# Kernel tuning notes

Hardware: AMD Instinct MI355X
Metric: run time of the kernel (lower is better)

The kernel has to match this reference:

```python
import jax, jax.numpy as jnp
import numpy as np

N_EMBD = 1024
N_HEAD = 16

def setup_inputs() -> dict:
    key = jax.random.key(0)
    ks = jax.random.split(key, 5)
    s = 0.02
    return {
        "x": jax.random.normal(ks[0], (4, 2048, N_EMBD), dtype=jnp.float32),
        "w_attn": jax.random.normal(ks[1], (N_EMBD, 3 * N_EMBD), dtype=jnp.float32) * s,
        "b_attn": jnp.zeros((3 * N_EMBD,), dtype=jnp.float32),
        "w_proj": jax.random.normal(ks[2], (N_EMBD, N_EMBD), dtype=jnp.float32) * s,
        "b_proj": jnp.zeros((N_EMBD,), dtype=jnp.float32),
    }

def reference(x, w_attn, b_attn, w_proj, b_proj):
    B, T, C = x.shape
    H = N_HEAD
    D = C // H
    qkv = x @ w_attn + b_attn                       # [B,T,3C]
    q, k, v = jnp.split(qkv, 3, axis=-1)
    # [B,H,T,D]
    q = q.reshape(B, T, H, D).transpose(0, 2, 1, 3)
    k = k.reshape(B, T, H, D).transpose(0, 2, 1, 3)
    v = v.reshape(B, T, H, D).transpose(0, 2, 1, 3)
    scale = 1.0 / jnp.sqrt(jnp.asarray(D, dtype=x.dtype))
    attn = jnp.einsum("bhqd,bhkd->bhqk", q, k) * scale
    mask = jnp.tril(jnp.ones((T, T), dtype=bool))
    attn = jnp.where(mask, attn, jnp.asarray(-jnp.inf, dtype=attn.dtype))
    attn = jax.nn.softmax(attn, axis=-1)
    out = jnp.einsum("bhqk,bhkd->bhqd", attn, v)    # [B,H,T,D]
    out = out.transpose(0, 2, 1, 3).reshape(B, T, C)
    return out @ w_proj + b_proj
```

## Files before the change

### kernel.cpp

```cpp
#include <hip/hip_runtime.h>


typedef unsigned short u16b;
typedef __bf16 bf16x8 __attribute__((ext_vector_type(8)));
typedef float f32x4 __attribute__((ext_vector_type(4)));
typedef float f32x16 __attribute__((ext_vector_type(16)));
typedef unsigned short u16x4 __attribute__((ext_vector_type(4)));

#define AS1(p) ((const __attribute__((address_space(1))) void*)(p))
#define AS3(p) ((__attribute__((address_space(3))) void*)(p))
#define GLDS(g, l) __builtin_amdgcn_global_load_lds(AS1(g), AS3(l), 16, 0, 0)

__device__ __forceinline__ u16b bfr(float v) {
  union { float f; unsigned u; } x; x.f = v;
  unsigned r = x.u + 0x7fffu + ((x.u >> 16) & 1u);
  return (u16b)(r >> 16);
}

__device__ __forceinline__ unsigned pk2(float lo, float hi) {
  union { __bf16 h[2]; unsigned u; } t;
  t.h[0] = (__bf16)lo; t.h[1] = (__bf16)hi;
  return t.u;
}

__device__ __forceinline__ float max16(const f32x16& v) {
  float a0 = fmaxf(v[0], v[1]), a1 = fmaxf(v[2], v[3]);
  float a2 = fmaxf(v[4], v[5]), a3 = fmaxf(v[6], v[7]);
  float b0 = fmaxf(v[8], v[9]), b1 = fmaxf(v[10], v[11]);
  float b2 = fmaxf(v[12], v[13]), b3 = fmaxf(v[14], v[15]);
  float c0 = fmaxf(a0, a1), c1 = fmaxf(a2, a3);
  float c2 = fmaxf(b0, b1), c3 = fmaxf(b2, b3);
  return fmaxf(fmaxf(c0, c1), fmaxf(c2, c3));
}

__device__ __forceinline__ float sum16(const f32x16& v) {
  float a0 = v[0] + v[1], a1 = v[2] + v[3], a2 = v[4] + v[5], a3 = v[6] + v[7];
  float b0 = v[8] + v[9], b1 = v[10] + v[11], b2 = v[12] + v[13], b3 = v[14] + v[15];
  float c0 = a0 + a1, c1 = a2 + a3, c2 = b0 + b1, c3 = b2 + b3;
  return (c0 + c1) + (c2 + c3);
}

__global__ __launch_bounds__(256) void cvt_bf16_kernel(
    const float* __restrict__ src, u16b* __restrict__ dst, int n4) {
  int i = blockIdx.x * 256 + threadIdx.x;
  const int stride = gridDim.x * 256;
  for (; i < n4; i += stride) {
    const float4 v = reinterpret_cast<const float4*>(src)[i];
    u16x4 o;
    o[0] = bfr(v.x); o[1] = bfr(v.y); o[2] = bfr(v.z); o[3] = bfr(v.w);
    reinterpret_cast<u16x4*>(dst)[i] = o;
  }
}

__global__ __launch_bounds__(256) void transpose_cvt_kernel(
    const float* __restrict__ src, u16b* __restrict__ dst, int R, int C) {
  __shared__ u16b tile[64][72];
  const int nc = C >> 6;
  const int br = blockIdx.x / nc, bc = blockIdx.x % nc;
  const int r0 = br << 6, c0 = bc << 6;
  const int c = threadIdx.x & 63, r4 = threadIdx.x >> 6;
  #pragma unroll
  for (int i = 0; i < 16; ++i) {
    const int r = r4 + 4 * i;
    tile[r][c] = bfr(src[(size_t)(r0 + r) * C + c0 + c]);
  }
  __syncthreads();
  #pragma unroll
  for (int i = 0; i < 16; ++i) {
    const int rr = r4 + 4 * i;
    dst[(size_t)(c0 + rr) * R + r0 + c] = tile[c][rr];
  }
}

template <int EPI>
__global__ __launch_bounds__(256, 2) void gemm128_kernel(
    const u16b* __restrict__ A, const u16b* __restrict__ Bt,
    const float* __restrict__ bias,
    u16b* __restrict__ oQ, u16b* __restrict__ oK, u16b* __restrict__ oVt,
    float* __restrict__ oF, int M, int N, int K) {
  __shared__ u16b smem[16384];
  const int tid = threadIdx.x;
  const int wid = tid >> 6, lane = tid & 63;
  const int nb = N >> 7;
  const int lin = (blockIdx.x & 7) * ((int)gridDim.x >> 3) + (blockIdx.x >> 3);
  const int brow = lin / nb, bcol = lin % nb;
  const int wr = (wid >> 1) << 6, wc = (wid & 1) << 6;

  f32x4 acc[4][4] = {};

  const int ar = (wid << 4) + (lane >> 2);
  const int acs = (((lane & 3) ^ ((lane >> 3) & 3))) << 3;
  const u16b* Ab = A + (size_t)((brow << 7) + ar) * K + acs;
  const u16b* Bb = Bt + (size_t)((bcol << 7) + ar) * K + acs;
  const int fr = lane & 15;
  const int pcs = (((lane >> 4) ^ ((fr >> 1) & 3))) << 4;
  const int nk = K >> 5;

#define STAGE(bufi, kk)                                                        \
  {                                                                            \
    char* sb = (char*)smem + (bufi) * 16384;                                   \
    GLDS(Ab + (kk),                  sb + wid * 1024);                         \
    GLDS(Ab + (size_t)64 * K + (kk), sb + 4096 + wid * 1024);                  \
    GLDS(Bb + (kk),                  sb + 8192 + wid * 1024);                  \
    GLDS(Bb + (size_t)64 * K + (kk), sb + 12288 + wid * 1024);                 \
  }

  STAGE(0, 0);
  STAGE(1, 32);

  #pragma unroll 1
  for (int kt = 0; kt < nk; ++kt) {
    if (kt + 1 < nk) asm volatile("s_waitcnt vmcnt(4)" ::: "memory");
    else             asm volatile("s_waitcnt vmcnt(0)" ::: "memory");
    __builtin_amdgcn_s_barrier();

    const char* As = (const char*)smem + (kt & 1) * 16384;
    const char* Bs = As + 8192;
    bf16x8 af[4], bfv[4];
    #pragma unroll
    for (int i = 0; i < 4; ++i)
      af[i] = *(const bf16x8*)(As + (wr + i * 16 + fr) * 64 + pcs);
    #pragma unroll
    for (int j = 0; j < 4; ++j)
      bfv[j] = *(const bf16x8*)(Bs + (wc + j * 16 + fr) * 64 + pcs);
    __builtin_amdgcn_s_setprio(1);
    #pragma unroll
    for (int i = 0; i < 4; ++i)
      #pragma unroll
      for (int j = 0; j < 4; ++j)
        acc[i][j] = __builtin_amdgcn_mfma_f32_16x16x32_bf16(af[i], bfv[j], acc[i][j], 0, 0, 0);
    __builtin_amdgcn_s_setprio(0);

    __builtin_amdgcn_s_barrier();
    if (kt + 2 < nk) STAGE(kt & 1, (kt + 2) << 5);
  }
#undef STAGE

  const int fq = lane >> 4;
  if (EPI == 1) {
    #pragma unroll
    for (int j = 0; j < 4; ++j) {
      const int n0 = (bcol << 7) + wc + j * 16 + fr;
      const float bv = bias[n0];
      #pragma unroll
      for (int i = 0; i < 4; ++i) {
        #pragma unroll
        for (int r = 0; r < 4; ++r) {
          const int m0 = (brow << 7) + wr + i * 16 + fq * 4 + r;
          oF[(size_t)m0 * N + n0] = acc[i][j][r] + bv;
        }
      }
    }
  } else {
    const int sect = bcol >> 3;
    if (sect < 2) {
      const float qs = (sect == 0) ? 0.1803368801f : 1.0f;
      u16b* oPtr = (sect == 0) ? oQ : oK;
      u16b* tile = (u16b*)smem;
      #pragma unroll
      for (int j = 0; j < 4; ++j) {
        const int n = wc + j * 16 + fr;
        const float bv = bias[(bcol << 7) + n];
        #pragma unroll
        for (int i = 0; i < 4; ++i) {
          #pragma unroll
          for (int r = 0; r < 4; ++r) {
            const int m = wr + i * 16 + fq * 4 + r;
            const int byteoff = m * 256 + (((n >> 3) ^ (m & 7)) << 4) + ((n & 7) << 1);
            *(u16b*)((char*)tile + byteoff) = bfr((acc[i][j][r] + bv) * qs);
          }
        }
      }
      __syncthreads();
      const int nh = wid >> 1;
      const int c = lane & 7;
      #pragma unroll
      for (int it = 0; it < 8; ++it) {
        const int m = ((wid & 1) << 6) + (it << 3) + (lane >> 3);
        const int chunk = (nh << 3) + (c ^ (m & 7));
        const bf16x8 val = *(const bf16x8*)((const char*)tile + m * 256 + chunk * 16);
        const int m0 = (brow << 7) + m;
        const int n0 = (bcol << 7) + (nh << 6) + (c << 3);
        const int bb = m0 >> 11, tt = m0 & 2047;
        const int h = (n0 >> 6) & 15, d = n0 & 63;
        *(bf16x8*)(oPtr + (((size_t)(bb * 16 + h) * 2048 + tt) * 64 + d)) = val;
      }
    } else {
      u16b* tile = (u16b*)smem;
      #pragma unroll
      for (int j = 0; j < 4; ++j) {
        const int nl = wc + j * 16 + fr;
        const float bv = bias[(bcol << 7) + nl];
        #pragma unroll
        for (int i = 0; i < 4; ++i) {
          #pragma unroll
          for (int r = 0; r < 4; ++r) {
            const int m = wr + i * 16 + fq * 4 + r;
            const int byteoff = nl * 256 + (((m >> 3) ^ (nl & 7)) << 4) + ((m & 7) << 1);
            *(u16b*)((char*)tile + byteoff) = bfr(acc[i][j][r] + bv);
          }
        }
      }
      __syncthreads();
      const int row0 = wid << 5;
      const int c16 = lane & 15;
      const int rr = lane >> 4;
      const int t0 = (brow << 7) & 2047;
      const int bb = brow >> 4;
      #pragma unroll
      for (int it = 0; it < 8; ++it) {
        const int nl = row0 + (it << 2) + rr;
        const int pch = c16 ^ (nl & 7);
        const bf16x8 val = *(const bf16x8*)((const char*)tile + nl * 256 + pch * 16);
        const int h = ((bcol & 7) << 1) + (nl >> 6);
        const int d = nl & 63;
        *(bf16x8*)(oVt + ((size_t)((bb << 4) + h) * 64 + d) * 2048 + t0 + (c16 << 3)) = val;
      }
    }
  }
}

__global__ __launch_bounds__(256, 2) void flash_kernel(
    const u16b* __restrict__ Q, const u16b* __restrict__ K,
    const u16b* __restrict__ Vt, u16b* __restrict__ O) {
  __shared__ u16b smem[32768];
  const int bid = blockIdx.x;
  const int bh = bid & 63;
  const int dp = bid >> 6;
  const int p = (dp < 4) ? dp : (11 - dp);
  const int g1 = p, g2 = 15 - p;
  const int tid = threadIdx.x, wid = tid >> 6, lane = tid & 63;
  const int ln31 = lane & 31, hi = lane >> 5;
  const int l7 = ln31 & 7;
  const size_t baseQK = (size_t)bh * 2048 * 64;
  const size_t baseV = (size_t)bh * 64 * 2048;
  const int b = bh >> 4, h = bh & 15;
  const int rk = lane >> 3;
  const int sk = ((lane & 7) ^ rk) << 3;
  const int rv = lane >> 4;
  const int cv = lane & 15;

#define FSTAGE(kt, bi)                                                         \
  {                                                                            \
    char* kb_ = (char*)smem + (bi) * 32768;                                    \
    char* vb_ = kb_ + 16384;                                                   \
    const int k0_ = (kt) << 7;                                                 \
    _Pragma("unroll")                                                          \
    for (int c = 0; c < 4; ++c) {                                              \
      const int i = 4 * wid + c;                                               \
      const int r = 8 * i + rk;                                                \
      GLDS(K + baseQK + (size_t)(k0_ + r) * 64 + sk, kb_ + i * 1024);          \
    }                                                                          \
    _Pragma("unroll")                                                          \
    for (int c = 0; c < 4; ++c) {                                              \
      const int i = 4 * wid + c;                                               \
      const int r = 4 * i + rv;                                                \
      const int scv = (cv ^ (r & 7)) << 3;                                     \
      GLDS(Vt + baseV + (size_t)r * 2048 + k0_ + scv, vb_ + i * 1024);         \
    }                                                                          \
  }

  const int q0wA = (g1 << 7) + wid * 32;
  const int q0wB = (g2 << 7) + wid * 32;

  bf16x8 qfA[4], qfB[4];
  {
    const u16b* qpA = Q + baseQK + (size_t)(q0wA + ln31) * 64 + hi * 8;
    const u16b* qpB = Q + baseQK + (size_t)(q0wB + ln31) * 64 + hi * 8;
    #pragma unroll
    for (int kk = 0; kk < 4; ++kk) {
      qfA[kk] = *(const bf16x8*)(qpA + kk * 16);
      qfB[kk] = *(const bf16x8*)(qpB + kk * 16);
    }
  }

  float mA = -3e38f, lA = 0.f, mB = -3e38f, lB = 0.f;
  f32x16 oaA0 = {}, oaA1 = {}, oaB0 = {}, oaB1 = {};

  FSTAGE(0, 0);
  FSTAGE(1, 1);

  #pragma unroll 1
  for (int kt = 0; kt <= g2; ++kt) {
    if (kt < g2) asm volatile("s_waitcnt vmcnt(8)" ::: "memory");
    else         asm volatile("s_waitcnt vmcnt(0)" ::: "memory");
    __builtin_amdgcn_s_barrier();

    const char* kb = (const char*)smem + (kt & 1) * 32768;
    const char* vb = kb + 16384;

    auto compute_tile = [&](const bf16x8* qf, float& m_run, float& l_run,
                            f32x16& oa0, f32x16& oa1, const int gq) {
      const bool diag = (kt == gq);
      const int maxsub = diag ? wid : 3;

      f32x16 s[4] = {};
      __builtin_amdgcn_s_setprio(1);
      #pragma unroll
      for (int ss = 0; ss < 4; ++ss) {
        if (ss <= maxsub) {
          const int row = 32 * ss + ln31;
          #pragma unroll
          for (int kk = 0; kk < 4; ++kk) {
            const int ch = (2 * kk + hi) ^ l7;
            const bf16x8 kf = *(const bf16x8*)(kb + row * 128 + ch * 16);
            s[ss] = __builtin_amdgcn_mfma_f32_32x32x16_bf16(kf, qf[kk], s[ss], 0, 0, 0);
          }
        }
      }
      __builtin_amdgcn_s_setprio(0);

      if (diag) {
        #pragma unroll
        for (int ss = 0; ss < 4; ++ss) {
          if (ss == wid) {
            #pragma unroll
            for (int r = 0; r < 16; ++r) {
              const int kvr = (r & 3) + 8 * (r >> 2) + 4 * hi;
              if (kvr > ln31) s[ss][r] = -3e38f;
            }
          }
        }
      }

      float tm = -3e38f;
      #pragma unroll
      for (int ss = 0; ss < 4; ++ss)
        if (ss <= maxsub) tm = fmaxf(tm, max16(s[ss]));
      tm = fmaxf(tm, __shfl_xor(tm, 32));

      if (!__all(tm <= m_run + 8.f)) {
        const float mnew = fmaxf(m_run, tm);
        const float scale = __builtin_amdgcn_exp2f(m_run - mnew);
        m_run = mnew;
        l_run *= scale;
        #pragma unroll
        for (int r = 0; r < 16; ++r) { oa0[r] *= scale; oa1[r] *= scale; }
      }

      float rs = 0.f;
      #pragma unroll
      for (int ss = 0; ss < 4; ++ss) {
        if (ss <= maxsub) {
          #pragma unroll
          for (int r = 0; r < 16; ++r)
            s[ss][r] = __builtin_amdgcn_exp2f(s[ss][r] - m_run);
          rs += sum16(s[ss]);
        }
      }
      rs += __shfl_xor(rs, 32);
      l_run += rs;

      union WB { unsigned u[4]; bf16x8 v; };
      __builtin_amdgcn_s_setprio(1);
      #pragma unroll
      for (int ss = 0; ss < 4; ++ss) {
        if (ss <= maxsub) {
          WB pA, pB;
#define MKPA(W0, W1, W2, W3, P0, P1, P2, P3, P4, P5, P6, P7)                 \
          {                                                                   \
            unsigned a0 = pk2(P0, P1), a1 = pk2(P2, P3);                      \
            unsigned b0 = pk2(P4, P5), b1 = pk2(P6, P7);                      \
            auto r0 = __builtin_amdgcn_permlane32_swap(a0, b0, false, false); \
            auto r1 = __builtin_amdgcn_permlane32_swap(a1, b1, false, false); \
            unsigned o0[2], o1[2];                                            \
            __builtin_memcpy(o0, &r0, 8); __builtin_memcpy(o1, &r1, 8);       \
            W0 = o0[0]; W2 = o0[1]; W1 = o1[0]; W3 = o1[1];                   \
          }
          MKPA(pA.u[0], pA.u[1], pA.u[2], pA.u[3],
               s[ss][0], s[ss][1], s[ss][2], s[ss][3],
               s[ss][4], s[ss][5], s[ss][6], s[ss][7]);
          MKPA(pB.u[0], pB.u[1], pB.u[2], pB.u[3],
               s[ss][8], s[ss][9], s[ss][10], s[ss][11],
               s[ss][12], s[ss][13], s[ss][14], s[ss][15]);
#undef MKPA
          const int cxa = ((4 * ss + hi) ^ l7) << 4;
          const int cxb = ((4 * ss + 2 + hi) ^ l7) << 4;
          const char* v0 = vb + ln31 * 256;
          const char* v1 = vb + (32 + ln31) * 256;
          oa0 = __builtin_amdgcn_mfma_f32_32x32x16_bf16(*(const bf16x8*)(v0 + cxa), pA.v, oa0, 0, 0, 0);
          oa1 = __builtin_amdgcn_mfma_f32_32x32x16_bf16(*(const bf16x8*)(v1 + cxa), pA.v, oa1, 0, 0, 0);
          oa0 = __builtin_amdgcn_mfma_f32_32x32x16_bf16(*(const bf16x8*)(v0 + cxb), pB.v, oa0, 0, 0, 0);
          oa1 = __builtin_amdgcn_mfma_f32_32x32x16_bf16(*(const bf16x8*)(v1 + cxb), pB.v, oa1, 0, 0, 0);
        }
      }
      __builtin_amdgcn_s_setprio(0);
    };

    compute_tile(qfB, mB, lB, oaB0, oaB1, g2);
    if (kt <= g1) compute_tile(qfA, mA, lA, oaA0, oaA1, g1);

    __builtin_amdgcn_s_barrier();
    if (kt + 2 <= g2) FSTAGE(kt + 2, kt & 1);
  }

  {
    const float inv = 1.0f / lA;
    const int q = q0wA + ln31;
    u16b* orow = O + (size_t)(b * 2048 + q) * 1024 + h * 64;
    #pragma unroll
    for (int rq = 0; rq < 4; ++rq) {
      u16x4 v0, v1;
      #pragma unroll
      for (int j = 0; j < 4; ++j) {
        v0[j] = bfr(oaA0[4 * rq + j] * inv);
        v1[j] = bfr(oaA1[4 * rq + j] * inv);
      }
      const int d0 = 8 * rq + 4 * hi;
      *(u16x4*)(orow + d0) = v0;
      *(u16x4*)(orow + 32 + d0) = v1;
    }
  }
  {
    const float inv = 1.0f / lB;
    const int q = q0wB + ln31;
    u16b* orow = O + (size_t)(b * 2048 + q) * 1024 + h * 64;
    #pragma unroll
    for (int rq = 0; rq < 4; ++rq) {
      u16x4 v0, v1;
      #pragma unroll
      for (int j = 0; j < 4; ++j) {
        v0[j] = bfr(oaB0[4 * rq + j] * inv);
        v1[j] = bfr(oaB1[4 * rq + j] * inv);
      }
      const int d0 = 8 * rq + 4 * hi;
      *(u16x4*)(orow + d0) = v0;
      *(u16x4*)(orow + 32 + d0) = v1;
    }
  }
#undef FSTAGE
}

extern "C" void kernel_launch(void* const* d_in, const int* in_sizes, int n_in,
                              void* d_out, int out_size, void* d_ws, size_t ws_size,
                              hipStream_t stream) {
  const float* x      = (const float*)d_in[0];
  const float* w_attn = (const float*)d_in[1];
  const float* b_attn = (const float*)d_in[2];
  const float* w_proj = (const float*)d_in[3];
  const float* b_proj = (const float*)d_in[4];
  float* out = (float*)d_out;
  char* ws = (char*)d_ws;

  u16b* xb  = (u16b*)(ws + 0);
  u16b* waT = (u16b*)(ws + 16777216);
  u16b* wpT = (u16b*)(ws + 23068672);
  u16b* Qb  = (u16b*)(ws + 25165824);
  u16b* Kb  = (u16b*)(ws + 41943040);
  u16b* Vtb = (u16b*)(ws + 75497472);
  u16b* attn = xb;

  cvt_bf16_kernel<<<2048, 256, 0, stream>>>(x, xb, (8192 * 1024) / 4);
  transpose_cvt_kernel<<<16 * 48, 256, 0, stream>>>(w_attn, waT, 1024, 3072);
  transpose_cvt_kernel<<<16 * 16, 256, 0, stream>>>(w_proj, wpT, 1024, 1024);
  gemm128_kernel<0><<<64 * 24, 256, 0, stream>>>(xb, waT, b_attn, Qb, Kb, Vtb, nullptr,
                                                 8192, 3072, 1024);
  flash_kernel<<<512, 256, 0, stream>>>(Qb, Kb, Vtb, attn);
  gemm128_kernel<1><<<64 * 8, 256, 0, stream>>>(attn, wpT, b_proj, nullptr, nullptr, nullptr,
                                                out, 8192, 1024, 1024);
}
```

Measured before the change: 172.0 us.

## Split flash attention into one query tile per block with 64-key KV tiles

Each flash block now handles a single 128-row query tile instead of a balanced pair of tiles. KV stages shrink from 128 to 64 keys, which halves shared memory and raises the occupancy target to 4 blocks per CU. The grid doubles to 1024 blocks, ordered so the longest causal tiles launch first. The aim is more concurrent waves for latency hiding and better load spreading, at the cost of more barriers and loop iterations per key range, and losing the explicit pairing balance. Some unused dead index variables are also left in the PV section.

```diff
diff --git a/kernel.cpp b/kernel.cpp
--- a/kernel.cpp
+++ b/kernel.cpp
@@ -220,89 +220,70 @@
   }
 }
 
-__global__ __launch_bounds__(256, 2) void flash_kernel(
+__global__ __launch_bounds__(256, 4) void flash_kernel(
     const u16b* __restrict__ Q, const u16b* __restrict__ K,
     const u16b* __restrict__ Vt, u16b* __restrict__ O) {
-  __shared__ u16b smem[32768];
+  __shared__ u16b smem[16384];
   const int bid = blockIdx.x;
   const int bh = bid & 63;
-  const int dp = bid >> 6;
-  const int p = (dp < 4) ? dp : (11 - dp);
-  const int g1 = p, g2 = 15 - p;
+  const int qt = 15 - (bid >> 6);
   const int tid = threadIdx.x, wid = tid >> 6, lane = tid & 63;
   const int ln31 = lane & 31, hi = lane >> 5;
   const int l7 = ln31 & 7;
   const size_t baseQK = (size_t)bh * 2048 * 64;
   const size_t baseV = (size_t)bh * 64 * 2048;
   const int b = bh >> 4, h = bh & 15;
-  const int rk = lane >> 3;
-  const int sk = ((lane & 7) ^ rk) << 3;
-  const int rv = lane >> 4;
-  const int cv = lane & 15;
+  const int srow = wid * 8 + (lane >> 3);
+  const int sc = ((lane & 7) ^ (srow & 7)) << 3;
+
+  const int q0w = (qt << 7) + wid * 32;
+  const int NT = 2 * qt + 2;
+  const int LT = q0w >> 6;
 
 #define FSTAGE(kt, bi)                                                         \
   {                                                                            \
-    char* kb_ = (char*)smem + (bi) * 32768;                                    \
-    char* vb_ = kb_ + 16384;                                                   \
-    const int k0_ = (kt) << 7;                                                 \
-    _Pragma("unroll")                                                          \
-    for (int c = 0; c < 4; ++c) {                                              \
-      const int i = 4 * wid + c;                                               \
-      const int r = 8 * i + rk;                                                \
-      GLDS(K + baseQK + (size_t)(k0_ + r) * 64 + sk, kb_ + i * 1024);          \
-    }                                                                          \
-    _Pragma("unroll")                                                          \
-    for (int c = 0; c < 4; ++c) {                                              \
-      const int i = 4 * wid + c;                                               \
-      const int r = 4 * i + rv;                                                \
-      const int scv = (cv ^ (r & 7)) << 3;                                     \
-      GLDS(Vt + baseV + (size_t)r * 2048 + k0_ + scv, vb_ + i * 1024);         \
-    }                                                                          \
-  }
-
-  const int q0wA = (g1 << 7) + wid * 32;
-  const int q0wB = (g2 << 7) + wid * 32;
-
-  bf16x8 qfA[4], qfB[4];
+    char* kb_ = (char*)smem + (bi) * 16384;                                    \
+    const int k0_ = (kt) << 6;                                                 \
+    GLDS(K + baseQK + (size_t)(k0_ + srow) * 64 + sc,        kb_ + wid * 1024);\
+    GLDS(K + baseQK + (size_t)(k0_ + 32 + srow) * 64 + sc,   kb_ + 4096 + wid * 1024);\
+    GLDS(Vt + baseV + (size_t)srow * 2048 + k0_ + sc,        kb_ + 8192 + wid * 1024);\
+    GLDS(Vt + baseV + (size_t)(32 + srow) * 2048 + k0_ + sc, kb_ + 12288 + wid * 1024);\
+  }
+
+  bf16x8 qf[4];
   {
-    const u16b* qpA = Q + baseQK + (size_t)(q0wA + ln31) * 64 + hi * 8;
-    const u16b* qpB = Q + baseQK + (size_t)(q0wB + ln31) * 64 + hi * 8;
-    #pragma unroll
-    for (int kk = 0; kk < 4; ++kk) {
-      qfA[kk] = *(const bf16x8*)(qpA + kk * 16);
-      qfB[kk] = *(const bf16x8*)(qpB + kk * 16);
-    }
-  }
-
-  float mA = -3e38f, lA = 0.f, mB = -3e38f, lB = 0.f;
-  f32x16 oaA0 = {}, oaA1 = {}, oaB0 = {}, oaB1 = {};
+    const u16b* qp = Q + baseQK + (size_t)(q0w + ln31) * 64 + hi * 8;
+    #pragma unroll
+    for (int kk = 0; kk < 4; ++kk) qf[kk] = *(const bf16x8*)(qp + kk * 16);
+  }
+
+  float m_run = -3e38f, l_run = 0.f;
+  f32x16 oa0 = {}, oa1 = {};
 
   FSTAGE(0, 0);
   FSTAGE(1, 1);
 
   #pragma unroll 1
-  for (int kt = 0; kt <= g2; ++kt) {
-    if (kt < g2) asm volatile("s_waitcnt vmcnt(8)" ::: "memory");
-    else         asm volatile("s_waitcnt vmcnt(0)" ::: "memory");
+  for (int kt = 0; kt < NT; ++kt) {
+    if (kt + 1 < NT) asm volatile("s_waitcnt vmcnt(4)" ::: "memory");
+    else             asm volatile("s_waitcnt vmcnt(0)" ::: "memory");
     __builtin_amdgcn_s_barrier();
 
-    const char* kb = (const char*)smem + (kt & 1) * 32768;
-    const char* vb = kb + 16384;
-
-    auto compute_tile = [&](const bf16x8* qf, float& m_run, float& l_run,
-                            f32x16& oa0, f32x16& oa1, const int gq) {
-      const bool diag = (kt == gq);
-      const int maxsub = diag ? wid : 3;
-
-      f32x16 s[4] = {};
+    if (kt <= LT) {
+      const char* kb = (const char*)smem + (kt & 1) * 16384;
+      const char* vb = kb + 8192;
+      const bool diag = (kt == LT);
+      const int maxsub = diag ? (wid & 1) : 1;
+
+      f32x16 s[2] = {};
       __builtin_amdgcn_s_setprio(1);
       #pragma unroll
-      for (int ss = 0; ss < 4; ++ss) {
+      for (int ss = 0; ss < 2; ++ss) {
         if (ss <= maxsub) {
           const int row = 32 * ss + ln31;
           #pragma unroll
           for (int kk = 0; kk < 4; ++kk) {
-            const int ch = (2 * kk + hi) ^ l7;
+            const int ch = (2 * kk + hi) ^ (row & 7);
             const bf16x8 kf = *(const bf16x8*)(kb + row * 128 + ch * 16);
             s[ss] = __builtin_amdgcn_mfma_f32_32x32x16_bf16(kf, qf[kk], s[ss], 0, 0, 0);
           }
@@ -312,8 +293,8 @@
 
       if (diag) {
         #pragma unroll
-        for (int ss = 0; ss < 4; ++ss) {
-          if (ss == wid) {
+        for (int ss = 0; ss < 2; ++ss) {
+          if (ss == (wid & 1)) {
             #pragma unroll
             for (int r = 0; r < 16; ++r) {
               const int kvr = (r & 3) + 8 * (r >> 2) + 4 * hi;
@@ -325,7 +306,7 @@
 
       float tm = -3e38f;
       #pragma unroll
-      for (int ss = 0; ss < 4; ++ss)
+      for (int ss = 0; ss < 2; ++ss)
         if (ss <= maxsub) tm = fmaxf(tm, max16(s[ss]));
       tm = fmaxf(tm, __shfl_xor(tm, 32));
 
@@ -340,7 +321,7 @@
 
       float rs = 0.f;
       #pragma unroll
-      for (int ss = 0; ss < 4; ++ss) {
+      for (int ss = 0; ss < 2; ++ss) {
         if (ss <= maxsub) {
           #pragma unroll
           for (int r = 0; r < 16; ++r)
@@ -354,7 +335,7 @@
       union WB { unsigned u[4]; bf16x8 v; };
       __builtin_amdgcn_s_setprio(1);
       #pragma unroll
-      for (int ss = 0; ss < 4; ++ss) {
+      for (int ss = 0; ss < 2; ++ss) {
         if (ss <= maxsub) {
           WB pA, pB;
 #define MKPA(W0, W1, W2, W3, P0, P1, P2, P3, P4, P5, P6, P7)                 \
@@ -374,59 +355,50 @@
                s[ss][8], s[ss][9], s[ss][10], s[ss][11],
                s[ss][12], s[ss][13], s[ss][14], s[ss][15]);
 #undef MKPA
-          const int cxa = ((4 * ss + hi) ^ l7) << 4;
-          const int cxb = ((4 * ss + 2 + hi) ^ l7) << 4;
-          const char* v0 = vb + ln31 * 256;
-          const char* v1 = vb + (32 + ln31) * 256;
-          oa0 = __builtin_amdgcn_mfma_f32_32x32x16_bf16(*(const bf16x8*)(v0 + cxa), pA.v, oa0, 0, 0, 0);
-          oa1 = __builtin_amdgcn_mfma_f32_32x32x16_bf16(*(const bf16x8*)(v1 + cxa), pA.v, oa1, 0, 0, 0);
-          oa0 = __builtin_amdgcn_mfma_f32_32x32x16_bf16(*(const bf16x8*)(v0 + cxb), pB.v, oa0, 0, 0, 0);
-          oa1 = __builtin_amdgcn_mfma_f32_32x32x16_bf16(*(const bf16x8*)(v1 + cxb), pB.v, oa1, 0, 0, 0);
+          const int r0v = ln31, r1v = 32 + ln31;
+          const int cxa0 = ((2 * ss + hi) ^ (r0v & 7)) << 4;
+          const int cxa1 = ((2 * ss + hi) ^ (r1v & 7)) << 4;
+          const int cxb0 = ((2 * ss + 1 - hi + hi * 1 + 0) , 0);
+          (void)cxb0;
+          const int cb0 = (((2 * (ss) + 0) , 0)); (void)cb0;
+          const int sl_b = 2 * ss + 1;
+          const int cxB0 = ((2 * sl_b + hi - 2 * ss - hi) , 0); (void)cxB0;
+          const int chB0 = ((2 * sl_b + hi) ^ (r0v & 7)) << 4;
+          const int chB1 = ((2 * sl_b + hi) ^ (r1v & 7)) << 4;
+          const char* v0 = vb + r0v * 128;
+          const char* v1 = vb + r1v * 128;
+          const int chA0 = ((4 * ss + hi) ^ (r0v & 7)) << 4;
+          const int chA1 = ((4 * ss + hi) ^ (r1v & 7)) << 4;
+          const int chBB0 = ((4 * ss + 2 + hi) ^ (r0v & 7)) << 4;
+          const int chBB1 = ((4 * ss + 2 + hi) ^ (r1v & 7)) << 4;
+          (void)cxa0; (void)cxa1; (void)chB0; (void)chB1;
+          oa0 = __builtin_amdgcn_mfma_f32_32x32x16_bf16(*(const bf16x8*)(v0 + chA0), pA.v, oa0, 0, 0, 0);
+          oa1 = __builtin_amdgcn_mfma_f32_32x32x16_bf16(*(const bf16x8*)(v1 + chA1), pA.v, oa1, 0, 0, 0);
+          oa0 = __builtin_amdgcn_mfma_f32_32x32x16_bf16(*(const bf16x8*)(v0 + chBB0), pB.v, oa0, 0, 0, 0);
+          oa1 = __builtin_amdgcn_mfma_f32_32x32x16_bf16(*(const bf16x8*)(v1 + chBB1), pB.v, oa1, 0, 0, 0);
         }
       }
       __builtin_amdgcn_s_setprio(0);
-    };
-
-    compute_tile(qfB, mB, lB, oaB0, oaB1, g2);
-    if (kt <= g1) compute_tile(qfA, mA, lA, oaA0, oaA1, g1);
+    }
 
     __builtin_amdgcn_s_barrier();
-    if (kt + 2 <= g2) FSTAGE(kt + 2, kt & 1);
-  }
-
-  {
-    const float inv = 1.0f / lA;
-    const int q = q0wA + ln31;
-    u16b* orow = O + (size_t)(b * 2048 + q) * 1024 + h * 64;
-    #pragma unroll
-    for (int rq = 0; rq < 4; ++rq) {
-      u16x4 v0, v1;
-      #pragma unroll
-      for (int j = 0; j < 4; ++j) {
-        v0[j] = bfr(oaA0[4 * rq + j] * inv);
-        v1[j] = bfr(oaA1[4 * rq + j] * inv);
-      }
-      const int d0 = 8 * rq + 4 * hi;
-      *(u16x4*)(orow + d0) = v0;
-      *(u16x4*)(orow + 32 + d0) = v1;
+    if (kt + 2 < NT) FSTAGE(kt + 2, kt & 1);
+  }
+
+  const float inv = 1.0f / l_run;
+  const int q = q0w + ln31;
+  u16b* orow = O + (size_t)(b * 2048 + q) * 1024 + h * 64;
+  #pragma unroll
+  for (int rq = 0; rq < 4; ++rq) {
+    u16x4 v0, v1;
+    #pragma unroll
+    for (int j = 0; j < 4; ++j) {
+      v0[j] = bfr(oa0[4 * rq + j] * inv);
+      v1[j] = bfr(oa1[4 * rq + j] * inv);
     }
-  }
-  {
-    const float inv = 1.0f / lB;
-    const int q = q0wB + ln31;
-    u16b* orow = O + (size_t)(b * 2048 + q) * 1024 + h * 64;
-    #pragma unroll
-    for (int rq = 0; rq < 4; ++rq) {
-      u16x4 v0, v1;
-      #pragma unroll
-      for (int j = 0; j < 4; ++j) {
-        v0[j] = bfr(oaB0[4 * rq + j] * inv);
-        v1[j] = bfr(oaB1[4 * rq + j] * inv);
-      }
-      const int d0 = 8 * rq + 4 * hi;
-      *(u16x4*)(orow + d0) = v0;
-      *(u16x4*)(orow + 32 + d0) = v1;
-    }
+    const int d0 = 8 * rq + 4 * hi;
+    *(u16x4*)(orow + d0) = v0;
+    *(u16x4*)(orow + 32 + d0) = v1;
   }
 #undef FSTAGE
 }
@@ -455,7 +427,7 @@
   transpose_cvt_kernel<<<16 * 16, 256, 0, stream>>>(w_proj, wpT, 1024, 1024);
   gemm128_kernel<0><<<64 * 24, 256, 0, stream>>>(xb, waT, b_attn, Qb, Kb, Vtb, nullptr,
                                                  8192, 3072, 1024);
-  flash_kernel<<<512, 256, 0, stream>>>(Qb, Kb, Vtb, attn);
+  flash_kernel<<<1024, 256, 0, stream>>>(Qb, Kb, Vtb, attn);
   gemm128_kernel<1><<<64 * 8, 256, 0, stream>>>(attn, wpT, b_proj, nullptr, nullptr, nullptr,
                                                 out, 8192, 1024, 1024);
 }
```

After: 175.5 us. +2.1%, slower.
